# Kernel optimization log

Measured on AMD Instinct MI355X. Metric: run time of the kernel, lower is better.

## Reference

```python
import jax, jax.numpy as jnp
import numpy as np

N = 4096
C = 128
L = 4
E = 131072
HEADS = 4
BN_EPS = 1e-5


def setup_inputs() -> dict:
    key = jax.random.key(0)
    ks = jax.random.split(key, 16)
    s = jnp.float32(0.05)

    def rn(k, shape):
        return jax.random.normal(k, shape, dtype=jnp.float32) * s

    return {
        "x": jax.random.normal(ks[0], (N, C), dtype=jnp.float32),
        "edge_index": jax.random.randint(ks[1], (2, E), 0, N, dtype=jnp.int64) if jax.config.read("jax_enable_x64") else jax.random.randint(ks[1], (2, E), 0, N, dtype=jnp.int32),
        "gin_w1": rn(ks[2], (L, C, C)), "gin_b1": jnp.zeros((L, C), jnp.float32),
        "gin_w2": rn(ks[3], (L, C, C)), "gin_b2": jnp.zeros((L, C), jnp.float32),
        "attn_in_w": rn(ks[4], (L, 3 * C, C)), "attn_in_b": jnp.zeros((L, 3 * C), jnp.float32),
        "attn_out_w": rn(ks[5], (L, C, C)), "attn_out_b": jnp.zeros((L, C), jnp.float32),
        "n1_g": jnp.ones((L, C), jnp.float32), "n1_b": jnp.zeros((L, C), jnp.float32),
        "n2_g": jnp.ones((L, C), jnp.float32), "n2_b": jnp.zeros((L, C), jnp.float32),
        "n3_g": jnp.ones((L, C), jnp.float32), "n3_b": jnp.zeros((L, C), jnp.float32),
        "mlp_w1": rn(ks[6], (L, 2 * C, C)), "mlp_b1": jnp.zeros((L, 2 * C), jnp.float32),
        "mlp_w2": rn(ks[7], (L, C, 2 * C)), "mlp_b2": jnp.zeros((L, C), jnp.float32),
        "head_w1": rn(ks[8], (C // 2, C)), "head_b1": jnp.zeros((C // 2,), jnp.float32),
        "head_w2": rn(ks[9], (C // 4, C // 2)), "head_b2": jnp.zeros((C // 4,), jnp.float32),
        "head_w3": rn(ks[10], (1, C // 4)), "head_b3": jnp.zeros((1,), jnp.float32),
    }


def _bn(x, g, b):
    # BatchNorm1d over the node dim, training-mode (biased var), eps=1e-5
    mu = x.mean(axis=0)
    var = x.var(axis=0)
    return g * (x - mu) * jax.lax.rsqrt(var + BN_EPS) + b


def _gin(x, src, dst, w1, b1, w2, b2):
    # GINConv with eps=0: nn(x + sum_{j in N(i)} x_j)
    agg = jax.ops.segment_sum(x[src], dst, num_segments=x.shape[0])
    h = x + agg
    h = jnp.maximum(h @ w1.T + b1, 0.0)
    return h @ w2.T + b2


def _mha(x, wi, bi, wo, bo):
    # torch.nn.MultiheadAttention self-attention over a single dense batch of N nodes
    n, c = x.shape
    d = c // HEADS
    q, k, v = jnp.split(x @ wi.T + bi, 3, axis=-1)
    q = q.reshape(n, HEADS, d)
    k = k.reshape(n, HEADS, d)
    v = v.reshape(n, HEADS, d)
    scores = jnp.einsum('nhd,mhd->hnm', q, k) / jnp.sqrt(jnp.asarray(d, x.dtype))
    a = jax.nn.softmax(scores, axis=-1)
    o = jnp.einsum('hnm,mhd->nhd', a, v).reshape(n, c)
    return o @ wo.T + bo


def _forward(x, edge_index, gin_w1, gin_b1, gin_w2, gin_b2, attn_in_w, attn_in_b,
             attn_out_w, attn_out_b, n1_g, n1_b, n2_g, n2_b, n3_g, n3_b,
             mlp_w1, mlp_b1, mlp_w2, mlp_b2, head_w1, head_b1, head_w2, head_b2,
             head_w3, head_b3):
    src, dst = edge_index[0], edge_index[1]
    for i in range(L):
        # local GIN branch + residual + batch norm
        h1 = _bn(_gin(x, src, dst, gin_w1[i], gin_b1[i], gin_w2[i], gin_b2[i]) + x, n1_g[i], n1_b[i])
        # global attention branch + residual + batch norm
        h2 = _bn(_mha(x, attn_in_w[i], attn_in_b[i], attn_out_w[i], attn_out_b[i]) + x, n2_g[i], n2_b[i])
        h = h1 + h2
        # GPSConv MLP (C -> 2C -> C) with residual and final batch norm
        m = jnp.maximum(h @ mlp_w1[i].T + mlp_b1[i], 0.0) @ mlp_w2[i].T + mlp_b2[i]
        x = _bn(h + m, n3_g[i], n3_b[i])
    # head MLP: C -> C/2 -> C/4 -> 1
    h = jnp.maximum(x @ head_w1.T + head_b1, 0.0)
    h = jnp.maximum(h @ head_w2.T + head_b2, 0.0)
    return h @ head_w3.T + head_b3


def reference(x, edge_index, gin_w1, gin_b1, gin_w2, gin_b2, attn_in_w, attn_in_b,
              attn_out_w, attn_out_b, n1_g, n1_b, n2_g, n2_b, n3_g, n3_b,
              mlp_w1, mlp_b1, mlp_w2, mlp_b2, head_w1, head_b1, head_w2, head_b2,
              head_w3, head_b3):
    return _forward(x, edge_index, gin_w1, gin_b1, gin_w2, gin_b2, attn_in_w, attn_in_b,
                    attn_out_w, attn_out_b, n1_g, n1_b, n2_g, n2_b, n3_g, n3_b,
                    mlp_w1, mlp_b1, mlp_w2, mlp_b2, head_w1, head_b1, head_w2, head_b2,
                    head_w3, head_b3)
```

## Files before the change

### kernel.cpp

```cpp
#include <hip/hip_runtime.h>

#define N_NODES 4096
#define C_DIM   128
#define L_LAYERS 4
#define E_EDGES 131072
#define H_HEADS 4
#define D_HEAD  32
#define NC      (N_NODES * C_DIM)
#define NCu     (N_NODES * C_DIM)
#define P_STRIDE 136
#define HS_STRIDE 152
#define T2S       264
#define AT_S      136

typedef short bf16x8 __attribute__((ext_vector_type(8)));
typedef float f32x4  __attribute__((ext_vector_type(4)));

__device__ __forceinline__ unsigned short f2bf(float f) {
    unsigned int u = __float_as_uint(f);
    u += 0x7fffu + ((u >> 16) & 1u);
    return (unsigned short)(u >> 16);
}

__device__ __forceinline__ float bf_lo(unsigned int u) { return __uint_as_float(u << 16); }
__device__ __forceinline__ float bf_hi(unsigned int u) { return __uint_as_float(u & 0xffff0000u); }

__device__ __forceinline__ bf16x8 pack8(const float* v) {
    bf16x8 o;
#pragma unroll
    for (int i = 0; i < 8; ++i) o[i] = (short)f2bf(v[i]);
    return o;
}

__global__ __launch_bounds__(256) void hist_kernel(const int* __restrict__ ei,
                                                   int* __restrict__ deg) {
    int e = blockIdx.x * 256 + threadIdx.x;
    atomicAdd(&deg[ei[E_EDGES + e]], 1);
}

__global__ __launch_bounds__(256) void scan_kernel(const int* __restrict__ deg,
                                                   int* __restrict__ rowstart,
                                                   int* __restrict__ cursor) {
    __shared__ int ts[256];
    const int tid = threadIdx.x;
    int loc[16];
    int s = 0;
#pragma unroll
    for (int i = 0; i < 16; ++i) { loc[i] = s; s += deg[tid * 16 + i]; }
    ts[tid] = s;
    __syncthreads();
    for (int off = 1; off < 256; off <<= 1) {
        int t = (tid >= off) ? ts[tid - off] : 0;
        __syncthreads();
        if (tid >= off) ts[tid] += t;
        __syncthreads();
    }
    int off0 = ts[tid] - s;
#pragma unroll
    for (int i = 0; i < 16; ++i) {
        int v = off0 + loc[i];
        rowstart[tid * 16 + i] = v;
        cursor[tid * 16 + i] = v;
    }
    if (tid == 255) rowstart[4096] = off0 + s;
}

__global__ __launch_bounds__(256) void fill_kernel(const int* __restrict__ ei,
                                                   int* __restrict__ cursor,
                                                   int* __restrict__ csr_src) {
    int e = blockIdx.x * 256 + threadIdx.x;
    int d = ei[E_EDGES + e];
    int s = ei[e];
    int p = atomicAdd(&cursor[d], 1);
    csr_src[p] = s;
}

__global__ __launch_bounds__(256) void wcvt(const float* __restrict__ s0, const float* __restrict__ s1,
                                            const float* __restrict__ s2, const float* __restrict__ s3,
                                            const float* __restrict__ s4, const float* __restrict__ s5,
                                            unsigned short* __restrict__ wbf) {
    int i0 = (blockIdx.x * 256 + threadIdx.x) * 8;
    const float* src; int base;
    if      (i0 < 65536)  { src = s0; base = 0; }
    else if (i0 < 131072) { src = s1; base = 65536; }
    else if (i0 < 327680) { src = s2; base = 131072; }
    else if (i0 < 393216) { src = s3; base = 327680; }
    else if (i0 < 524288) { src = s4; base = 393216; }
    else                  { src = s5; base = 524288; }
    const float* p = src + (i0 - base);
    float t[8];
#pragma unroll
    for (int i = 0; i < 8; ++i) t[i] = p[i];
    *(bf16x8*)(wbf + i0) = pack8(t);
}

__global__ __launch_bounds__(256, 8) void qkv_gather(const float* __restrict__ xprev,
                                                     const float* __restrict__ st3,
                                                     const float* __restrict__ g3p,
                                                     const float* __restrict__ b3p,
                                                     const unsigned short* __restrict__ Wbf,
                                                     const float* __restrict__ bias,
                                                     unsigned short* __restrict__ Qb,
                                                     unsigned short* __restrict__ Kb,
                                                     unsigned short* __restrict__ VT,
                                                     const int* __restrict__ rowstart,
                                                     const int* __restrict__ csr_src,
                                                     float* __restrict__ ssz,
                                                     unsigned int* __restrict__ hsum) {
    __shared__ float scl2[2][128];
    __shared__ __align__(16) unsigned short at[16 * AT_S];

    const int b = blockIdx.x;
    const int tid = threadIdx.x;
    const float inv_n = 1.f / N_NODES;

    if (b < 1536) {
        const int ct = b % 6, rt = b / 6;
        const int rowbase = rt * 16;

        if (tid < 128) {
            float sc = 1.f, sh = 0.f;
            if (st3) {
                float m = st3[tid] * inv_n;
                float vv = st3[128 + tid] * inv_n - m * m;
                float r = rsqrtf(vv + 1e-5f);
                sc = g3p[tid] * r;
                sh = b3p[tid] - m * sc;
            }
            scl2[0][tid] = sc; scl2[1][tid] = sh;
        }
        __syncthreads();

        {
            const int e0 = tid * 8;
            const int r = e0 >> 7, c = e0 & 127;
            const float* xp = xprev + (size_t)(rowbase + r) * 128 + c;
            float t[8];
#pragma unroll
            for (int i = 0; i < 8; ++i) t[i] = xp[i] * scl2[0][c + i] + scl2[1][c + i];
            *(bf16x8*)(&at[r * AT_S + c]) = pack8(t);
        }
        __syncthreads();

        const int wv = tid >> 6;
        const int lane = tid & 63, lg = lane >> 4, ll = lane & 15;
        const int colbase = ct * 64 + wv * 16;
        const unsigned short* Wp = Wbf + (size_t)(colbase + ll) * 128 + lg * 8;

        f32x4 acc = {0.f, 0.f, 0.f, 0.f};
#pragma unroll
        for (int k = 0; k < 128; k += 32) {
            bf16x8 a = *(const bf16x8*)(&at[ll * AT_S + k + lg * 8]);
            bf16x8 w = *(const bf16x8*)(Wp + k);
            acc = __builtin_amdgcn_mfma_f32_16x16x32_bf16(a, w, acc, 0, 0, 0);
        }

        const float qsc = 0.25506973f;
        const int col = colbase + ll;
        const float bi = bias[col];
#pragma unroll
        for (int r = 0; r < 4; ++r) {
            const int row = rowbase + lg * 4 + r;
            float v = acc[r] + bi;
            if (col < 128) {
                int hh = col >> 5, d = col & 31;
                Qb[((size_t)hh * N_NODES + row) * D_HEAD + d] = f2bf(v * qsc);
            } else if (col < 256) {
                int c2 = col - 128, hh = c2 >> 5, d = c2 & 31;
                Kb[((size_t)hh * N_NODES + row) * D_HEAD + d] = f2bf(v);
            } else {
                int c2 = col - 256, hh = c2 >> 5, d = c2 & 31;
                VT[((size_t)hh * D_HEAD + d) * N_NODES + row] = f2bf(v);
            }
        }
    } else {
        if (b == 1536) {
            ssz[tid] = 0.f; ssz[256 + tid] = 0.f; ssz[512 + tid] = 0.f;
        }
        const int node = (b - 1536) * 4 + (tid >> 6);
        const int lane = tid & 63;
        const int ch0 = lane * 2, ch1 = ch0 + 1;
        float sc0 = 1.f, sh0 = 0.f, sc1 = 1.f, sh1 = 0.f;
        if (st3) {
            float m0 = st3[ch0] * inv_n;
            float v0 = st3[128 + ch0] * inv_n - m0 * m0;
            float r0 = rsqrtf(v0 + 1e-5f);
            sc0 = g3p[ch0] * r0; sh0 = b3p[ch0] - m0 * sc0;
            float m1 = st3[ch1] * inv_n;
            float v1 = st3[128 + ch1] * inv_n - m1 * m1;
            float r1 = rsqrtf(v1 + 1e-5f);
            sc1 = g3p[ch1] * r1; sh1 = b3p[ch1] - m1 * sc1;
        }
        const int beg = rowstart[node], end = rowstart[node + 1];
        float2 sv = *(const float2*)(xprev + (size_t)node * 128 + ch0);
        float ax = sv.x * sc0 + sh0, ay = sv.y * sc1 + sh1;
        float bx = 0.f, by = 0.f;
        int e = beg;
        for (; e + 4 <= end; e += 4) {
            int s0 = csr_src[e], s1 = csr_src[e + 1], s2 = csr_src[e + 2], s3 = csr_src[e + 3];
            float2 v0 = *(const float2*)(xprev + (size_t)s0 * 128 + ch0);
            float2 v1 = *(const float2*)(xprev + (size_t)s1 * 128 + ch0);
            float2 v2 = *(const float2*)(xprev + (size_t)s2 * 128 + ch0);
            float2 v3 = *(const float2*)(xprev + (size_t)s3 * 128 + ch0);
            ax += (v0.x * sc0 + sh0) + (v1.x * sc0 + sh0);
            ay += (v0.y * sc1 + sh1) + (v1.y * sc1 + sh1);
            bx += (v2.x * sc0 + sh0) + (v3.x * sc0 + sh0);
            by += (v2.y * sc1 + sh1) + (v3.y * sc1 + sh1);
        }
        for (; e < end; ++e) {
            float2 v0 = *(const float2*)(xprev + (size_t)csr_src[e] * 128 + ch0);
            ax += v0.x * sc0 + sh0; ay += v0.y * sc1 + sh1;
        }
        float ox = ax + bx, oy = ay + by;
        hsum[(size_t)node * 64 + lane] = (unsigned int)f2bf(ox) | ((unsigned int)f2bf(oy) << 16);
    }
}

__global__ __launch_bounds__(512, 4) void attn_gin1(const unsigned short* __restrict__ Qb,
                                                    const unsigned short* __restrict__ Kb,
                                                    const unsigned short* __restrict__ VT,
                                                    unsigned short* __restrict__ ob,
                                                    const unsigned short* __restrict__ hsum,
                                                    const unsigned short* __restrict__ W1,
                                                    const float* __restrict__ bias1,
                                                    unsigned short* __restrict__ t1out) {
    __shared__ __align__(16) unsigned short Pl[8 * 32 * P_STRIDE];
    float (*Ouns)[32][33] = (float (*)[32][33])(void*)Pl;
    float (*Llp)[32] = (float (*)[32])(void*)(Pl + 8 * 32 * 33 * 2);

    const int b   = blockIdx.x;
    const int tid = threadIdx.x;
    const int wv  = tid >> 6;
    const int lane = tid & 63;
    const int lg  = lane >> 4;
    const int ll  = lane & 15;

    if (b >= 512) {
        const int rowbase = (b - 512) * 16;
        const int colbase = wv * 16;
        const unsigned short* Ap = hsum + (size_t)(rowbase + ll) * 128 + lg * 8;
        const unsigned short* Wp = W1 + (size_t)(colbase + ll) * 128 + lg * 8;
        f32x4 acc = {0.f, 0.f, 0.f, 0.f};
#pragma unroll
        for (int k = 0; k < 128; k += 32) {
            bf16x8 a = *(const bf16x8*)(Ap + k);
            bf16x8 w = *(const bf16x8*)(Wp + k);
            acc = __builtin_amdgcn_mfma_f32_16x16x32_bf16(a, w, acc, 0, 0, 0);
        }
        const int col = colbase + ll;
        const float bi = bias1[col];
#pragma unroll
        for (int r = 0; r < 4; ++r) {
            const int row = rowbase + lg * 4 + r;
            float v = fmaxf(acc[r] + bi, 0.f);
            t1out[(size_t)row * 128 + col] = f2bf(v);
        }
        return;
    }

    const int h   = b >> 7;
    const int q0  = (b & 127) * 32;

    const unsigned short* Qh = Qb + ((size_t)h * N_NODES + q0) * D_HEAD;
    const unsigned short* Kh = Kb + (size_t)h * N_NODES * D_HEAD;
    const unsigned short* Vh = VT + (size_t)h * D_HEAD * N_NODES;

    bf16x8 qf0 = *(const bf16x8*)(Qh + ll * D_HEAD + lg * 8);
    bf16x8 qf1 = *(const bf16x8*)(Qh + (16 + ll) * D_HEAD + lg * 8);

    f32x4 oacc00 = {0.f,0.f,0.f,0.f}, oacc01 = {0.f,0.f,0.f,0.f};
    f32x4 oacc10 = {0.f,0.f,0.f,0.f}, oacc11 = {0.f,0.f,0.f,0.f};
    float l0[4] = {0.f,0.f,0.f,0.f}, l1[4] = {0.f,0.f,0.f,0.f};

    unsigned short* Pw = Pl + wv * (32 * P_STRIDE);
    const int k0 = wv * (N_NODES / 8);

    for (int t = 0; t < (N_NODES / 8) / 128; ++t) {
        const int kt = k0 + t * 128;

        float s0[8][4], s1[8][4];
#pragma unroll
        for (int kc = 0; kc < 8; ++kc) {
            bf16x8 kf = *(const bf16x8*)(Kh + (size_t)(kt + kc * 16 + ll) * D_HEAD + lg * 8);
            f32x4 z = {0.f, 0.f, 0.f, 0.f};
            f32x4 d0 = __builtin_amdgcn_mfma_f32_16x16x32_bf16(qf0, kf, z, 0, 0, 0);
            f32x4 d1 = __builtin_amdgcn_mfma_f32_16x16x32_bf16(qf1, kf, z, 0, 0, 0);
#pragma unroll
            for (int r = 0; r < 4; ++r) { s0[kc][r] = d0[r]; s1[kc][r] = d1[r]; }
        }

#pragma unroll
        for (int r = 0; r < 4; ++r) {
            float a = 0.f, bb = 0.f;
#pragma unroll
            for (int kc = 0; kc < 8; ++kc) {
                float p0 = exp2f(s0[kc][r]); s0[kc][r] = p0; a += p0;
                float p1 = exp2f(s1[kc][r]); s1[kc][r] = p1; bb += p1;
            }
#pragma unroll
            for (int off = 1; off < 16; off <<= 1) {
                a += __shfl_xor(a, off, 64);
                bb += __shfl_xor(bb, off, 64);
            }
            l0[r] += a;
            l1[r] += bb;
        }

#pragma unroll
        for (int kc = 0; kc < 8; ++kc)
#pragma unroll
            for (int r = 0; r < 4; ++r) {
                Pw[(lg * 4 + r) * P_STRIDE + kc * 16 + ll]      = f2bf(s0[kc][r]);
                Pw[(16 + lg * 4 + r) * P_STRIDE + kc * 16 + ll] = f2bf(s1[kc][r]);
            }
        asm volatile("" ::: "memory");

#pragma unroll
        for (int kc2 = 0; kc2 < 4; ++kc2) {
            bf16x8 va = *(const bf16x8*)(Vh + (size_t)ll * N_NODES + kt + kc2 * 32 + lg * 8);
            bf16x8 vb = *(const bf16x8*)(Vh + (size_t)(16 + ll) * N_NODES + kt + kc2 * 32 + lg * 8);
            bf16x8 pf0 = *(const bf16x8*)(Pw + ll * P_STRIDE + kc2 * 32 + lg * 8);
            bf16x8 pf1 = *(const bf16x8*)(Pw + (16 + ll) * P_STRIDE + kc2 * 32 + lg * 8);
            oacc00 = __builtin_amdgcn_mfma_f32_16x16x32_bf16(pf0, va, oacc00, 0, 0, 0);
            oacc01 = __builtin_amdgcn_mfma_f32_16x16x32_bf16(pf0, vb, oacc01, 0, 0, 0);
            oacc10 = __builtin_amdgcn_mfma_f32_16x16x32_bf16(pf1, va, oacc10, 0, 0, 0);
            oacc11 = __builtin_amdgcn_mfma_f32_16x16x32_bf16(pf1, vb, oacc11, 0, 0, 0);
        }
    }

    __syncthreads();

#pragma unroll
    for (int r = 0; r < 4; ++r) {
        Ouns[wv][lg * 4 + r][ll]           = oacc00[r];
        Ouns[wv][lg * 4 + r][16 + ll]      = oacc01[r];
        Ouns[wv][16 + lg * 4 + r][ll]      = oacc10[r];
        Ouns[wv][16 + lg * 4 + r][16 + ll] = oacc11[r];
    }
    if (ll == 0) {
#pragma unroll
        for (int r = 0; r < 4; ++r) {
            Llp[wv][lg * 4 + r]      = l0[r];
            Llp[wv][16 + lg * 4 + r] = l1[r];
        }
    }
    __syncthreads();

    {
        const int row = tid >> 4, col = tid & 15;
        float L = 0.f, oa = 0.f, obv = 0.f;
#pragma unroll
        for (int w = 0; w < 8; ++w) {
            L   += Llp[w][row];
            oa  += Ouns[w][row][col];
            obv += Ouns[w][row][16 + col];
        }
        float inv = 1.f / L;
        ob[(size_t)(q0 + row) * C_DIM + h * D_HEAD + col]      = f2bf(oa * inv);
        ob[(size_t)(q0 + row) * C_DIM + h * D_HEAD + 16 + col] = f2bf(obv * inv);
    }
}

__global__ __launch_bounds__(256, 8) void gemm2x(const unsigned short* __restrict__ A0,
                                                 const unsigned short* __restrict__ W0,
                                                 const float* __restrict__ bias0,
                                                 float* __restrict__ out0,
                                                 float* __restrict__ stats0,
                                                 const unsigned short* __restrict__ A1,
                                                 const unsigned short* __restrict__ W1,
                                                 const float* __restrict__ bias1,
                                                 float* __restrict__ out1,
                                                 float* __restrict__ stats1,
                                                 const float* __restrict__ xprev,
                                                 const float* __restrict__ st3,
                                                 const float* __restrict__ g3p,
                                                 const float* __restrict__ b3p) {
    const int b = blockIdx.x;
    const int which = b >> 9;
    const int bl = b & 511;
    const unsigned short* Abf = which ? A1 : A0;
    const unsigned short* Wbf = which ? W1 : W0;
    const float* bias = which ? bias1 : bias0;
    float* outf  = which ? out1 : out0;
    float* stats = which ? stats1 : stats0;

    const int tid = threadIdx.x;
    const int wv = tid >> 6;
    const int lane = tid & 63, lg = lane >> 4, ll = lane & 15;
    const int rowbase = (bl >> 1) * 16;
    const int colbase = (bl & 1) * 64 + wv * 16;

    const unsigned short* Ap = Abf + (size_t)(rowbase + ll) * 128 + lg * 8;
    const unsigned short* Wp = Wbf + (size_t)(colbase + ll) * 128 + lg * 8;

    f32x4 acc = {0.f, 0.f, 0.f, 0.f};
#pragma unroll
    for (int k = 0; k < 128; k += 32) {
        bf16x8 a = *(const bf16x8*)(Ap + k);
        bf16x8 w = *(const bf16x8*)(Wp + k);
        acc = __builtin_amdgcn_mfma_f32_16x16x32_bf16(a, w, acc, 0, 0, 0);
    }

    const int col = colbase + ll;
    const float bi = bias[col];
    float sc = 1.f, sh = 0.f;
    if (st3) {
        const float inv_n = 1.f / N_NODES;
        float m = st3[col] * inv_n;
        float vv = st3[128 + col] * inv_n - m * m;
        float r = rsqrtf(vv + 1e-5f);
        sc = g3p[col] * r; sh = b3p[col] - m * sc;
    }
    float sv = 0.f, sv2 = 0.f;
#pragma unroll
    for (int r = 0; r < 4; ++r) {
        const int row = rowbase + lg * 4 + r;
        float v = acc[r] + bi + (xprev[(size_t)row * 128 + col] * sc + sh);
        outf[(size_t)row * 128 + col] = v;
        sv += v; sv2 += v * v;
    }
    sv  += __shfl_xor(sv, 16, 64);  sv  += __shfl_xor(sv, 32, 64);
    sv2 += __shfl_xor(sv2, 16, 64); sv2 += __shfl_xor(sv2, 32, 64);
    if (lg == 0) {
        atomicAdd(&stats[col], sv);
        atomicAdd(&stats[128 + col], sv2);
    }
}

__global__ __launch_bounds__(256) void mlp_fused(const float* __restrict__ g1p,
                                                 const float* __restrict__ a2p,
                                                 const float* __restrict__ st1,
                                                 const float* __restrict__ st2,
                                                 const float* __restrict__ g1v,
                                                 const float* __restrict__ b1v,
                                                 const float* __restrict__ g2v,
                                                 const float* __restrict__ b2v,
                                                 const unsigned short* __restrict__ W1bf,
                                                 const float* __restrict__ bias1,
                                                 const unsigned short* __restrict__ W2bf,
                                                 const float* __restrict__ bias2,
                                                 float* __restrict__ m3out,
                                                 float* __restrict__ stats3) {
    __shared__ float hf[16][132];
    __shared__ __align__(16) unsigned short hs[16 * HS_STRIDE];
    __shared__ __align__(16) unsigned short t2s[16 * T2S];
    __shared__ float scl[4][128];

    const int tid = threadIdx.x;
    const int rowbase = blockIdx.x * 16;
    const float inv_n = 1.f / N_NODES;

    if (tid < 128) {
        const int ch = tid;
        float m1 = st1[ch] * inv_n;
        float v1 = st1[128 + ch] * inv_n - m1 * m1;
        float r1 = rsqrtf(v1 + 1e-5f);
        float sc1 = g1v[ch] * r1;
        scl[0][ch] = sc1;
        scl[1][ch] = b1v[ch] - m1 * sc1;
        float m2 = st2[ch] * inv_n;
        float v2 = st2[128 + ch] * inv_n - m2 * m2;
        float r2 = rsqrtf(v2 + 1e-5f);
        float sc2 = g2v[ch] * r2;
        scl[2][ch] = sc2;
        scl[3][ch] = b2v[ch] - m2 * sc2;
    }
    __syncthreads();

#pragma unroll
    for (int j = tid; j < 512; j += 256) {
        const int r = j >> 5, cq = (j & 31) * 4;
        float4 v1 = *(const float4*)(g1p + (size_t)(rowbase + r) * 128 + cq);
        float4 v2 = *(const float4*)(a2p + (size_t)(rowbase + r) * 128 + cq);
        float h0 = v1.x * scl[0][cq]     + scl[1][cq]     + v2.x * scl[2][cq]     + scl[3][cq];
        float h1 = v1.y * scl[0][cq + 1] + scl[1][cq + 1] + v2.y * scl[2][cq + 1] + scl[3][cq + 1];
        float h2 = v1.z * scl[0][cq + 2] + scl[1][cq + 2] + v2.z * scl[2][cq + 2] + scl[3][cq + 2];
        float h3 = v1.w * scl[0][cq + 3] + scl[1][cq + 3] + v2.w * scl[2][cq + 3] + scl[3][cq + 3];
        hf[r][cq] = h0; hf[r][cq + 1] = h1; hf[r][cq + 2] = h2; hf[r][cq + 3] = h3;
        ushort4 u;
        u.x = f2bf(h0); u.y = f2bf(h1); u.z = f2bf(h2); u.w = f2bf(h3);
        *(ushort4*)(&hs[r * HS_STRIDE + cq]) = u;
    }
    __syncthreads();

    const int wv = tid >> 6;
    const int lane = tid & 63, lg = lane >> 4, ll = lane & 15;

#pragma unroll
    for (int ct = 0; ct < 4; ++ct) {
        const int colbase = wv * 16 + ct * 64;
        const unsigned short* Wp = W1bf + (size_t)(colbase + ll) * 128 + lg * 8;
        f32x4 acc = {0.f, 0.f, 0.f, 0.f};
#pragma unroll
        for (int k = 0; k < 128; k += 32) {
            bf16x8 a = *(const bf16x8*)(&hs[ll * HS_STRIDE + k + lg * 8]);
            bf16x8 w = *(const bf16x8*)(Wp + k);
            acc = __builtin_amdgcn_mfma_f32_16x16x32_bf16(a, w, acc, 0, 0, 0);
        }
        const int col = colbase + ll;
        const float bi = bias1[col];
#pragma unroll
        for (int r = 0; r < 4; ++r) {
            float v = fmaxf(acc[r] + bi, 0.f);
            t2s[(lg * 4 + r) * T2S + col] = f2bf(v);
        }
    }
    __syncthreads();

#pragma unroll
    for (int p = 0; p < 2; ++p) {
        const int colbase = p * 64 + wv * 16;
        const unsigned short* Wp = W2bf + (size_t)(colbase + ll) * 256 + lg * 8;
        f32x4 acc = {0.f, 0.f, 0.f, 0.f};
#pragma unroll
        for (int k = 0; k < 256; k += 32) {
            bf16x8 a = *(const bf16x8*)(&t2s[ll * T2S + k + lg * 8]);
            bf16x8 w = *(const bf16x8*)(Wp + k);
            acc = __builtin_amdgcn_mfma_f32_16x16x32_bf16(a, w, acc, 0, 0, 0);
        }
        const int col = colbase + ll;
        const float bi = bias2[col];
        float sv = 0.f, sv2 = 0.f;
#pragma unroll
        for (int r = 0; r < 4; ++r) {
            const int row = lg * 4 + r;
            float v = acc[r] + bi + hf[row][col];
            m3out[(size_t)(rowbase + row) * 128 + col] = v;
            sv += v; sv2 += v * v;
        }
        sv  += __shfl_xor(sv, 16, 64);  sv  += __shfl_xor(sv, 32, 64);
        sv2 += __shfl_xor(sv2, 16, 64); sv2 += __shfl_xor(sv2, 32, 64);
        if (lg == 0) {
            atomicAdd(&stats3[col], sv);
            atomicAdd(&stats3[128 + col], sv2);
        }
    }
}

__global__ __launch_bounds__(256) void head_fused(const float* __restrict__ m3p,
                                                  const float* __restrict__ st3,
                                                  const float* __restrict__ g3p,
                                                  const float* __restrict__ b3p,
                                                  const float* __restrict__ w1,
                                                  const float* __restrict__ b1,
                                                  const float* __restrict__ w2,
                                                  const float* __restrict__ b2,
                                                  const float* __restrict__ w3,
                                                  const float* __restrict__ b3,
                                                  float* __restrict__ out) {
    __shared__ __align__(16) float xs[8][128];
    __shared__ __align__(16) float hs2[8][64];
    __shared__ float scl2[2][128];
    const int tid = threadIdx.x;
    const int n = tid >> 5;
    const int g = tid & 31;
    const int node0 = blockIdx.x * 8;
    const float inv_n = 1.f / N_NODES;

    if (tid < 128) {
        float m = st3[tid] * inv_n;
        float vv = st3[128 + tid] * inv_n - m * m;
        float r = rsqrtf(vv + 1e-5f);
        float sc = g3p[tid] * r;
        scl2[0][tid] = sc;
        scl2[1][tid] = b3p[tid] - m * sc;
    }
    __syncthreads();

    {
        const int e0 = tid * 4;
        const int r = e0 >> 7, c = e0 & 127;
        float4 v = *(const float4*)(m3p + (size_t)(node0 + r) * 128 + c);
        xs[r][c]     = v.x * scl2[0][c]     + scl2[1][c];
        xs[r][c + 1] = v.y * scl2[0][c + 1] + scl2[1][c + 1];
        xs[r][c + 2] = v.z * scl2[0][c + 2] + scl2[1][c + 2];
        xs[r][c + 3] = v.w * scl2[0][c + 3] + scl2[1][c + 3];
    }
    __syncthreads();

    {
        float acc0 = b1[g], acc1 = b1[g + 32];
        const float* wa = w1 + (size_t)g * 128;
        const float* wb = w1 + (size_t)(g + 32) * 128;
#pragma unroll 8
        for (int k = 0; k < 128; k += 4) {
            float4 xv = *(const float4*)(&xs[n][k]);
            float4 va = *(const float4*)(wa + k);
            float4 vb = *(const float4*)(wb + k);
            acc0 += xv.x * va.x + xv.y * va.y + xv.z * va.z + xv.w * va.w;
            acc1 += xv.x * vb.x + xv.y * vb.y + xv.z * vb.z + xv.w * vb.w;
        }
        hs2[n][g]      = fmaxf(acc0, 0.f);
        hs2[n][g + 32] = fmaxf(acc1, 0.f);
    }
    __syncthreads();

    {
        float acc = b2[g];
        const float* wr = w2 + (size_t)g * 64;
#pragma unroll 8
        for (int k = 0; k < 64; k += 4) {
            float4 hv = *(const float4*)(&hs2[n][k]);
            float4 wv = *(const float4*)(wr + k);
            acc += hv.x * wv.x + hv.y * wv.y + hv.z * wv.z + hv.w * wv.w;
        }
        float t = fmaxf(acc, 0.f) * w3[g];
#pragma unroll
        for (int off = 1; off < 32; off <<= 1) t += __shfl_xor(t, off, 64);
        if (g == 0) out[node0 + n] = t + b3[0];
    }
}

extern "C" void kernel_launch(void* const* d_in, const int* in_sizes, int n_in,
                              void* d_out, int out_size, void* d_ws, size_t ws_size,
                              hipStream_t stream) {
    (void)in_sizes; (void)n_in; (void)out_size; (void)ws_size;
    const float* x_in   = (const float*)d_in[0];
    const int*   ei     = (const int*)d_in[1];
    const float* gin_w1 = (const float*)d_in[2];
    const float* gin_b1 = (const float*)d_in[3];
    const float* gin_w2 = (const float*)d_in[4];
    const float* gin_b2 = (const float*)d_in[5];
    const float* ain_w  = (const float*)d_in[6];
    const float* ain_b  = (const float*)d_in[7];
    const float* aout_w = (const float*)d_in[8];
    const float* aout_b = (const float*)d_in[9];
    const float* n1_g   = (const float*)d_in[10];
    const float* n1_b   = (const float*)d_in[11];
    const float* n2_g   = (const float*)d_in[12];
    const float* n2_b   = (const float*)d_in[13];
    const float* n3_g   = (const float*)d_in[14];
    const float* n3_b   = (const float*)d_in[15];
    const float* mlp_w1 = (const float*)d_in[16];
    const float* mlp_b1 = (const float*)d_in[17];
    const float* mlp_w2 = (const float*)d_in[18];
    const float* mlp_b2 = (const float*)d_in[19];
    const float* h_w1   = (const float*)d_in[20];
    const float* h_b1   = (const float*)d_in[21];
    const float* h_w2   = (const float*)d_in[22];
    const float* h_b2   = (const float*)d_in[23];
    const float* h_w3   = (const float*)d_in[24];
    const float* h_b3   = (const float*)d_in[25];

    float* f = (float*)d_ws;
    float* g1   = f;
    float* a2   = f + 1 * (size_t)NC;
    float* t1ch = f + 2 * (size_t)NC;
    float* m3   = f + 3 * (size_t)NC;
    unsigned short* R1  = (unsigned short*)(f + 4 * (size_t)NC);
    unsigned short* Qb      = R1;
    unsigned short* Kb      = R1 + (size_t)NCu;
    unsigned short* VT      = R1 + 2 * (size_t)NCu;
    unsigned short* R2      = R1 + 3 * (size_t)NCu;
    unsigned short* ao_bf   = R2;
    unsigned short* hsum_bf = (unsigned short*)a2;
    unsigned short* t1_bf   = (unsigned short*)t1ch;
    unsigned short* wbf     = R2 + (size_t)NCu;
    float* ssA    = (float*)(wbf + 655360);
    float* ssB    = ssA + 768;
    int* ibase    = (int*)(ssB + 768);
    int* deg      = ibase;
    int* rowstart = ibase + 4096;
    int* cursor   = ibase + 4096 + 4098;
    int* csr_src  = ibase + 4096 + 4098 + 4096;

    const int OG1 = 0, OG2 = 65536, OAI = 131072, OAO = 327680, OM1 = 393216, OM2 = 524288;

    hipMemsetAsync(deg, 0, 4096 * sizeof(int), stream);
    hist_kernel<<<E_EDGES / 256, 256, 0, stream>>>(ei, deg);
    scan_kernel<<<1, 256, 0, stream>>>(deg, rowstart, cursor);
    fill_kernel<<<E_EDGES / 256, 256, 0, stream>>>(ei, cursor, csr_src);
    wcvt<<<320, 256, 0, stream>>>(gin_w1, gin_w2, ain_w, aout_w, mlp_w1, mlp_w2, wbf);

    for (int i = 0; i < L_LAYERS; ++i) {
        const float* xprev = (i == 0) ? x_in : m3;
        const float* st3p  = (i == 0) ? nullptr : ((i & 1) ? ssA : ssB) + 512;
        const float* g3p   = (i == 0) ? nullptr : n3_g + (size_t)(i - 1) * C_DIM;
        const float* b3p   = (i == 0) ? nullptr : n3_b + (size_t)(i - 1) * C_DIM;
        float* ss_cur = (i & 1) ? ssB : ssA;
        const float* gb1 = gin_b1 + (size_t)i * C_DIM;
        const float* gb2 = gin_b2 + (size_t)i * C_DIM;
        const float* aib = ain_b + (size_t)i * 3 * C_DIM;
        const float* aob = aout_b + (size_t)i * C_DIM;
        const float* mb1 = mlp_b1 + (size_t)i * 2 * C_DIM;
        const float* mb2 = mlp_b2 + (size_t)i * C_DIM;

        qkv_gather<<<2560, 256, 0, stream>>>(xprev, st3p, g3p, b3p,
                                             wbf + OAI + (size_t)i * 49152, aib,
                                             Qb, Kb, VT, rowstart, csr_src,
                                             ss_cur, (unsigned int*)hsum_bf);
        attn_gin1<<<768, 512, 0, stream>>>(Qb, Kb, VT, ao_bf,
                                           hsum_bf, wbf + OG1 + (size_t)i * 16384, gb1, t1_bf);
        gemm2x<<<1024, 256, 0, stream>>>(t1_bf, wbf + OG2 + (size_t)i * 16384, gb2, g1, ss_cur,
                                         ao_bf, wbf + OAO + (size_t)i * 16384, aob, a2, ss_cur + 256,
                                         xprev, st3p, g3p, b3p);
        mlp_fused<<<256, 256, 0, stream>>>(g1, a2, ss_cur, ss_cur + 256,
                                           n1_g + (size_t)i * C_DIM, n1_b + (size_t)i * C_DIM,
                                           n2_g + (size_t)i * C_DIM, n2_b + (size_t)i * C_DIM,
                                           wbf + OM1 + (size_t)i * 32768, mb1,
                                           wbf + OM2 + (size_t)i * 32768, mb2,
                                           m3, ss_cur + 512);
    }

    head_fused<<<N_NODES / 8, 256, 0, stream>>>(m3, ssB + 512,
                                                n3_g + 3 * (size_t)C_DIM, n3_b + 3 * (size_t)C_DIM,
                                                h_w1, h_b1, h_w2, h_b2, h_w3, h_b3,
                                                (float*)d_out);
}
```

Before: 366.8 us.

## Stream attention P tiles in 32-key chunks to cut LDS and registers

The attention loop now computes scores, exponentiates and writes P in 32-key chunks into a small per-wave LDS tile (stride 40) that aliases the output-reduction buffer, instead of holding a full 128-key tile in registers and LDS. The row-sum shuffle reduction is deferred to after the key loop rather than done every tile. Launch bounds rise to 8 blocks per CU, aiming for higher occupancy from less LDS and fewer registers. In exchange, more barriers and smaller MFMA batches per step may reduce instruction-level parallelism.

```diff
diff --git a/kernel.cpp b/kernel.cpp
--- a/kernel.cpp
+++ b/kernel.cpp
@@ -8,7 +8,7 @@
 #define D_HEAD  32
 #define NC      (N_NODES * C_DIM)
 #define NCu     (N_NODES * C_DIM)
-#define P_STRIDE 136
+#define P2S     40
 #define HS_STRIDE 152
 #define T2S       264
 #define AT_S      136
@@ -216,7 +216,7 @@
     }
 }
 
-__global__ __launch_bounds__(512, 4) void attn_gin1(const unsigned short* __restrict__ Qb,
+__global__ __launch_bounds__(512, 8) void attn_gin1(const unsigned short* __restrict__ Qb,
                                                     const unsigned short* __restrict__ Kb,
                                                     const unsigned short* __restrict__ VT,
                                                     unsigned short* __restrict__ ob,
@@ -224,9 +224,8 @@
                                                     const unsigned short* __restrict__ W1,
                                                     const float* __restrict__ bias1,
                                                     unsigned short* __restrict__ t1out) {
-    __shared__ __align__(16) unsigned short Pl[8 * 32 * P_STRIDE];
-    float (*Ouns)[32][33] = (float (*)[32][33])(void*)Pl;
-    float (*Llp)[32] = (float (*)[32])(void*)(Pl + 8 * 32 * 33 * 2);
+    __shared__ __align__(16) float Ouns[8][32][33];
+    __shared__ float Llp[8][32];
 
     const int b   = blockIdx.x;
     const int tid = threadIdx.x;
@@ -268,74 +267,66 @@
     bf16x8 qf0 = *(const bf16x8*)(Qh + ll * D_HEAD + lg * 8);
     bf16x8 qf1 = *(const bf16x8*)(Qh + (16 + ll) * D_HEAD + lg * 8);
 
-    f32x4 oacc00 = {0.f,0.f,0.f,0.f}, oacc01 = {0.f,0.f,0.f,0.f};
-    f32x4 oacc10 = {0.f,0.f,0.f,0.f}, oacc11 = {0.f,0.f,0.f,0.f};
+    f32x4 o00 = {0.f,0.f,0.f,0.f}, o01 = {0.f,0.f,0.f,0.f};
+    f32x4 o10 = {0.f,0.f,0.f,0.f}, o11 = {0.f,0.f,0.f,0.f};
     float l0[4] = {0.f,0.f,0.f,0.f}, l1[4] = {0.f,0.f,0.f,0.f};
 
-    unsigned short* Pw = Pl + wv * (32 * P_STRIDE);
+    unsigned short* Pw = (unsigned short*)(void*)Ouns + wv * (32 * P2S);
     const int k0 = wv * (N_NODES / 8);
+    const unsigned short* Vrow_lo = Vh + (size_t)ll * N_NODES;
+    const unsigned short* Vrow_hi = Vh + (size_t)(16 + ll) * N_NODES;
 
     for (int t = 0; t < (N_NODES / 8) / 128; ++t) {
         const int kt = k0 + t * 128;
-
-        float s0[8][4], s1[8][4];
-#pragma unroll
-        for (int kc = 0; kc < 8; ++kc) {
-            bf16x8 kf = *(const bf16x8*)(Kh + (size_t)(kt + kc * 16 + ll) * D_HEAD + lg * 8);
-            f32x4 z = {0.f, 0.f, 0.f, 0.f};
-            f32x4 d0 = __builtin_amdgcn_mfma_f32_16x16x32_bf16(qf0, kf, z, 0, 0, 0);
-            f32x4 d1 = __builtin_amdgcn_mfma_f32_16x16x32_bf16(qf1, kf, z, 0, 0, 0);
-#pragma unroll
-            for (int r = 0; r < 4; ++r) { s0[kc][r] = d0[r]; s1[kc][r] = d1[r]; }
-        }
-
-#pragma unroll
-        for (int r = 0; r < 4; ++r) {
-            float a = 0.f, bb = 0.f;
-#pragma unroll
-            for (int kc = 0; kc < 8; ++kc) {
-                float p0 = exp2f(s0[kc][r]); s0[kc][r] = p0; a += p0;
-                float p1 = exp2f(s1[kc][r]); s1[kc][r] = p1; bb += p1;
+#pragma unroll
+        for (int j = 0; j < 4; ++j) {
+#pragma unroll
+            for (int w = 0; w < 2; ++w) {
+                const int kc = 2 * j + w;
+                bf16x8 kf = *(const bf16x8*)(Kh + (size_t)(kt + kc * 16 + ll) * D_HEAD + lg * 8);
+                f32x4 z = {0.f, 0.f, 0.f, 0.f};
+                f32x4 d0 = __builtin_amdgcn_mfma_f32_16x16x32_bf16(qf0, kf, z, 0, 0, 0);
+                f32x4 d1 = __builtin_amdgcn_mfma_f32_16x16x32_bf16(qf1, kf, z, 0, 0, 0);
+#pragma unroll
+                for (int r = 0; r < 4; ++r) {
+                    float p0 = exp2f(d0[r]); l0[r] += p0;
+                    float p1 = exp2f(d1[r]); l1[r] += p1;
+                    Pw[(lg * 4 + r) * P2S + w * 16 + ll]      = f2bf(p0);
+                    Pw[(16 + lg * 4 + r) * P2S + w * 16 + ll] = f2bf(p1);
+                }
             }
-#pragma unroll
-            for (int off = 1; off < 16; off <<= 1) {
-                a += __shfl_xor(a, off, 64);
-                bb += __shfl_xor(bb, off, 64);
-            }
-            l0[r] += a;
-            l1[r] += bb;
-        }
-
-#pragma unroll
-        for (int kc = 0; kc < 8; ++kc)
-#pragma unroll
-            for (int r = 0; r < 4; ++r) {
-                Pw[(lg * 4 + r) * P_STRIDE + kc * 16 + ll]      = f2bf(s0[kc][r]);
-                Pw[(16 + lg * 4 + r) * P_STRIDE + kc * 16 + ll] = f2bf(s1[kc][r]);
-            }
-        asm volatile("" ::: "memory");
-
-#pragma unroll
-        for (int kc2 = 0; kc2 < 4; ++kc2) {
-            bf16x8 va = *(const bf16x8*)(Vh + (size_t)ll * N_NODES + kt + kc2 * 32 + lg * 8);
-            bf16x8 vb = *(const bf16x8*)(Vh + (size_t)(16 + ll) * N_NODES + kt + kc2 * 32 + lg * 8);
-            bf16x8 pf0 = *(const bf16x8*)(Pw + ll * P_STRIDE + kc2 * 32 + lg * 8);
-            bf16x8 pf1 = *(const bf16x8*)(Pw + (16 + ll) * P_STRIDE + kc2 * 32 + lg * 8);
-            oacc00 = __builtin_amdgcn_mfma_f32_16x16x32_bf16(pf0, va, oacc00, 0, 0, 0);
-            oacc01 = __builtin_amdgcn_mfma_f32_16x16x32_bf16(pf0, vb, oacc01, 0, 0, 0);
-            oacc10 = __builtin_amdgcn_mfma_f32_16x16x32_bf16(pf1, va, oacc10, 0, 0, 0);
-            oacc11 = __builtin_amdgcn_mfma_f32_16x16x32_bf16(pf1, vb, oacc11, 0, 0, 0);
-        }
-    }
-
-    __syncthreads();
+            asm volatile("" ::: "memory");
+
+            const int kb = kt + 32 * j + lg * 8;
+            bf16x8 va = *(const bf16x8*)(Vrow_lo + kb);
+            bf16x8 vb = *(const bf16x8*)(Vrow_hi + kb);
+            bf16x8 pf0 = *(const bf16x8*)(Pw + ll * P2S + lg * 8);
+            bf16x8 pf1 = *(const bf16x8*)(Pw + (16 + ll) * P2S + lg * 8);
+            o00 = __builtin_amdgcn_mfma_f32_16x16x32_bf16(pf0, va, o00, 0, 0, 0);
+            o01 = __builtin_amdgcn_mfma_f32_16x16x32_bf16(pf0, vb, o01, 0, 0, 0);
+            o10 = __builtin_amdgcn_mfma_f32_16x16x32_bf16(pf1, va, o10, 0, 0, 0);
+            o11 = __builtin_amdgcn_mfma_f32_16x16x32_bf16(pf1, vb, o11, 0, 0, 0);
+            asm volatile("" ::: "memory");
+        }
+    }
 
 #pragma unroll
     for (int r = 0; r < 4; ++r) {
-        Ouns[wv][lg * 4 + r][ll]           = oacc00[r];
-        Ouns[wv][lg * 4 + r][16 + ll]      = oacc01[r];
-        Ouns[wv][16 + lg * 4 + r][ll]      = oacc10[r];
-        Ouns[wv][16 + lg * 4 + r][16 + ll] = oacc11[r];
+#pragma unroll
+        for (int off = 1; off < 16; off <<= 1) {
+            l0[r] += __shfl_xor(l0[r], off, 64);
+            l1[r] += __shfl_xor(l1[r], off, 64);
+        }
+    }
+
+    __syncthreads();
+
+#pragma unroll
+    for (int r = 0; r < 4; ++r) {
+        Ouns[wv][lg * 4 + r][ll]           = o00[r];
+        Ouns[wv][lg * 4 + r][16 + ll]      = o01[r];
+        Ouns[wv][16 + lg * 4 + r][ll]      = o10[r];
+        Ouns[wv][16 + lg * 4 + r][16 + ll] = o11[r];
     }
     if (ll == 0) {
 #pragma unroll
```

Result: slower. 627.4 us (+71.0%).
